# Kernel optimization log

Hardware: AMD Instinct MI355X
Metric: run time of the kernel (lower is better)

## Reference

```python
import jax, jax.numpy as jnp
import numpy as np
from jax import lax

VOCAB = 12000
EMB = 512
RNN = 512
FEATS = 4096
SEQ_LEN = 15


def setup_inputs() -> dict:
    key = jax.random.key(0)
    ks = jax.random.split(key, 10)
    B = 1024
    s = 0.05
    return {
        "img_features": jax.random.normal(ks[0], (B, FEATS), jnp.float32),
        "W_feats": jax.random.normal(ks[1], (EMB, FEATS), jnp.float32) * s,
        "b_feats": jax.random.normal(ks[2], (EMB,), jnp.float32) * s,
        "W_ih": jax.random.normal(ks[3], (4 * RNN, EMB), jnp.float32) * s,
        "W_hh": jax.random.normal(ks[4], (4 * RNN, RNN), jnp.float32) * s,
        "b_ih": jax.random.normal(ks[5], (4 * RNN,), jnp.float32) * s,
        "b_hh": jax.random.normal(ks[6], (4 * RNN,), jnp.float32) * s,
        "emb": jax.random.normal(ks[7], (VOCAB, EMB), jnp.float32) * s,
        "W_out": jax.random.normal(ks[8], (VOCAB - 2, RNN), jnp.float32) * s,
        "b_out": jax.random.normal(ks[9], (VOCAB - 2,), jnp.float32) * s,
    }


def reference(img_features, W_feats, b_feats, W_ih, W_hh, b_ih, b_hh, emb, W_out, b_out):
    B = img_features.shape[0]

    def lstm_cell(x, h, c):
        # torch.nn.LSTMCell: gates ordered i, f, g, o
        gates = x @ W_ih.T + b_ih + h @ W_hh.T + b_hh
        i, f, g, o = jnp.split(gates, 4, axis=1)
        c_new = jax.nn.sigmoid(f) * c + jax.nn.sigmoid(i) * jnp.tanh(g)
        h_new = jax.nn.sigmoid(o) * jnp.tanh(c_new)
        return h_new, c_new

    # image feature embedding + ReLU, then prime the LSTM with it
    img_vec = jax.nn.relu(img_features @ W_feats.T + b_feats)  # [B, 512]
    h = jnp.zeros((B, RNN), img_features.dtype)
    c = jnp.zeros((B, RNN), img_features.dtype)
    h, c = lstm_cell(img_vec, h, c)

    def step(carry, _):
        h, c, words = carry
        x = emb[words]                     # [B, 512] embedding lookup
        h, c = lstm_cell(x, h, c)
        logits = h @ W_out.T + b_out       # [B, VOCAB-2]
        idx = jnp.argmax(logits, axis=1).astype(jnp.int32)
        return (h, c, idx + 2), idx

    words0 = jnp.ones((B,), jnp.int32)  # START token = 1
    _, seq = lax.scan(step, (h, c, words0), None, length=SEQ_LEN)
    return seq.T  # [B, SEQ_LEN] greedy-decoded token ids
```

## Files before the change

### kernel.cpp

```cpp
#include <hip/hip_runtime.h>
#include <stdint.h>

#define BATCH  1024
#define SEQLEN 15
#define NGATE  2048
#define NVOCAB 11998
#define FEATS  4096

typedef __attribute__((ext_vector_type(8)))  short  s8v;
typedef __attribute__((ext_vector_type(16))) float  f32x16;
typedef __attribute__((ext_vector_type(8)))  unsigned short us8;

__device__ __forceinline__ unsigned short f2bf(float f) {
    unsigned u = __float_as_uint(f);
    u += 0x7FFFu + ((u >> 16) & 1u);
    return (unsigned short)(u >> 16);
}
__device__ __forceinline__ float bf2f(unsigned short h) {
    return __uint_as_float(((unsigned)h) << 16);
}
struct bfpair { unsigned short hi, lo; };
__device__ __forceinline__ bfpair split2v(float v) {
    bfpair r;
    r.hi = f2bf(v);
    r.lo = f2bf(v - bf2f(r.hi));
    return r;
}
__device__ __forceinline__ void split8(const float* __restrict__ s, us8& vh, us8& vl) {
    #pragma unroll
    for (int e = 0; e < 8; ++e) {
        bfpair q = split2v(s[e]);
        vh[e] = q.hi; vl[e] = q.lo;
    }
}

__device__ __forceinline__ void async_cp16(const void* g, void* l) {
    __builtin_amdgcn_global_load_lds(
        (const __attribute__((address_space(1))) unsigned int*)g,
        (__attribute__((address_space(3))) unsigned int*)l, 16, 0, 0);
}

__global__ void prep_wcat_blk(const float* __restrict__ W_ih, const float* __restrict__ W_hh,
                              const float* __restrict__ b_ih, const float* __restrict__ b_hh,
                              unsigned short* __restrict__ hi, unsigned short* __restrict__ lo,
                              float* __restrict__ bsum) {
    int idx = blockIdx.x * 256 + threadIdx.x;
    int kc = idx >> 11, row = idx & 2047;
    int k = kc << 3;
    const float* src = (k < 512) ? (W_ih + (size_t)row * 512 + k)
                                 : (W_hh + (size_t)row * 512 + (k - 512));
    us8 vh, vl; split8(src, vh, vl);
    *(us8*)(hi + (size_t)idx * 8) = vh;
    *(us8*)(lo + (size_t)idx * 8) = vl;
    if (idx < NGATE) bsum[idx] = b_ih[idx] + b_hh[idx];
}

__global__ void prep_blk(const float* __restrict__ src,
                         unsigned short* __restrict__ hi, unsigned short* __restrict__ lo,
                         int R, int K) {
    int row = blockIdx.x * 256 + threadIdx.x;
    if (row >= R) return;
    int kc = blockIdx.y;
    us8 vh, vl; split8(src + (size_t)row * K + (kc << 3), vh, vl);
    size_t o = ((size_t)kc * R + row) * 8;
    *(us8*)(hi + o) = vh;
    *(us8*)(lo + o) = vl;
}

__device__ __forceinline__ void mfma_blk_store(
    const unsigned short* __restrict__ Ahi, const unsigned short* __restrict__ Alo, int aRows,
    const unsigned short* __restrict__ Bhi, const unsigned short* __restrict__ Blo, int bRows,
    float* __restrict__ C, int ldc,
    int K, size_t akstride, size_t bkstride, size_t czstride)
{
    __shared__ short smem[4 * 4 * 128 * 8];
    short* sAhi = smem;
    short* sAlo = smem + 4 * 128 * 8;
    short* sBhi = smem + 2 * 4 * 128 * 8;
    short* sBlo = smem + 3 * 4 * 128 * 8;

    const int kz = blockIdx.z;
    Ahi += (size_t)kz * akstride;  Alo += (size_t)kz * akstride;
    Bhi += (size_t)kz * bkstride;  Blo += (size_t)kz * bkstride;
    C   += (size_t)kz * czstride;

    const int tid  = threadIdx.x;
    const int lane = tid & 63, wave = tid >> 6;
    const int wr = (wave & 1) * 64, wc = (wave >> 1) * 64;
    const int col = lane & 31, kh = lane >> 5;
    const int bm = blockIdx.y * 128, bn = blockIdx.x * 128;

    f32x16 acc[2][2] = {};

    for (int k0 = 0; k0 < K; k0 += 32) {
        const int kc0 = k0 >> 3;
        __syncthreads();
        #pragma unroll
        for (int p = 0; p < 2; ++p) {
            int s    = p * 4 + wave;
            int kc_l = s >> 1, rh = s & 1;
            int rl   = rh * 64 + lane;
            int lo_  = (kc_l * 128 + rh * 64) * 8;
            size_t ga = ((size_t)(kc0 + kc_l) * aRows + (bm + rl)) * 8;
            async_cp16(Ahi + ga, sAhi + lo_);
            async_cp16(Alo + ga, sAlo + lo_);
            int brow = bn + rl; if (brow > bRows - 1) brow = bRows - 1;
            size_t gb = ((size_t)(kc0 + kc_l) * bRows + brow) * 8;
            async_cp16(Bhi + gb, sBhi + lo_);
            async_cp16(Blo + gb, sBlo + lo_);
        }
        __syncthreads();

        #pragma unroll
        for (int st = 0; st < 2; ++st) {
            int off = (2 * st + kh) * 128 * 8;
            s8v ah0 = *(const s8v*)(sAhi + off + (wr + col) * 8);
            s8v ah1 = *(const s8v*)(sAhi + off + (wr + 32 + col) * 8);
            s8v al0 = *(const s8v*)(sAlo + off + (wr + col) * 8);
            s8v al1 = *(const s8v*)(sAlo + off + (wr + 32 + col) * 8);
            s8v bh0 = *(const s8v*)(sBhi + off + (wc + col) * 8);
            s8v bh1 = *(const s8v*)(sBhi + off + (wc + 32 + col) * 8);
            s8v bl0 = *(const s8v*)(sBlo + off + (wc + col) * 8);
            s8v bl1 = *(const s8v*)(sBlo + off + (wc + 32 + col) * 8);
            acc[0][0] = __builtin_amdgcn_mfma_f32_32x32x16_bf16(ah0, bh0, acc[0][0], 0, 0, 0);
            acc[0][1] = __builtin_amdgcn_mfma_f32_32x32x16_bf16(ah0, bh1, acc[0][1], 0, 0, 0);
            acc[1][0] = __builtin_amdgcn_mfma_f32_32x32x16_bf16(ah1, bh0, acc[1][0], 0, 0, 0);
            acc[1][1] = __builtin_amdgcn_mfma_f32_32x32x16_bf16(ah1, bh1, acc[1][1], 0, 0, 0);
            acc[0][0] = __builtin_amdgcn_mfma_f32_32x32x16_bf16(ah0, bl0, acc[0][0], 0, 0, 0);
            acc[0][1] = __builtin_amdgcn_mfma_f32_32x32x16_bf16(ah0, bl1, acc[0][1], 0, 0, 0);
            acc[1][0] = __builtin_amdgcn_mfma_f32_32x32x16_bf16(ah1, bl0, acc[1][0], 0, 0, 0);
            acc[1][1] = __builtin_amdgcn_mfma_f32_32x32x16_bf16(ah1, bl1, acc[1][1], 0, 0, 0);
            acc[0][0] = __builtin_amdgcn_mfma_f32_32x32x16_bf16(al0, bh0, acc[0][0], 0, 0, 0);
            acc[0][1] = __builtin_amdgcn_mfma_f32_32x32x16_bf16(al0, bh1, acc[0][1], 0, 0, 0);
            acc[1][0] = __builtin_amdgcn_mfma_f32_32x32x16_bf16(al1, bh0, acc[1][0], 0, 0, 0);
            acc[1][1] = __builtin_amdgcn_mfma_f32_32x32x16_bf16(al1, bh1, acc[1][1], 0, 0, 0);
        }
    }

    #pragma unroll
    for (int i = 0; i < 2; ++i)
        #pragma unroll
        for (int rg = 0; rg < 4; ++rg)
            #pragma unroll
            for (int rr = 0; rr < 4; ++rr) {
                int reg = rg * 4 + rr;
                int m = bm + wr + i * 32 + rr + rg * 8 + kh * 4;
                #pragma unroll
                for (int j = 0; j < 2; ++j) {
                    int n = bn + wc + j * 32 + col;
                    if (n < bRows) C[(size_t)m * ldc + n] = acc[i][j][reg];
                }
            }
}

__global__ __launch_bounds__(256) void k_gemm_gates(
    const unsigned short* Ahi, const unsigned short* Alo,
    const unsigned short* Bhi, const unsigned short* Blo,
    float* C, size_t aks, size_t bks, size_t czs) {
    mfma_blk_store(Ahi, Alo, 1024, Bhi, Blo, NGATE, C, NGATE, 512, aks, bks, czs);
}
__global__ __launch_bounds__(256) void k_gemm_feats(
    const unsigned short* Ahi, const unsigned short* Alo,
    const unsigned short* Bhi, const unsigned short* Blo,
    float* C) {
    mfma_blk_store(Ahi, Alo, 1024, Bhi, Blo, 512, C, 512, 512,
                   (size_t)64 * 1024 * 8, (size_t)64 * 512 * 8, (size_t)1024 * 512);
}

__global__ __launch_bounds__(128, 2) void k_logits_argmax(
    const unsigned short* __restrict__ h_hi, const unsigned short* __restrict__ h_lo,
    const unsigned short* __restrict__ wout_hi, const unsigned short* __restrict__ wout_lo,
    const float* __restrict__ bias, unsigned long long* __restrict__ packed) {
    __shared__ short smem[4 * 4 * 128 * 8];
    short* sAhi = smem;
    short* sAlo = smem + 4096;
    short* sBhi = smem + 8192;
    short* sBlo = smem + 12288;

    const int tid = threadIdx.x;
    const int lane = tid & 63, wave = tid >> 6;
    const int wr = wave * 64;
    const int col = lane & 31, kh = lane >> 5;
    const int bm = blockIdx.y * 128, bn = blockIdx.x * 128;
    const int aRows = 1024, bRows = NVOCAB;

    f32x16 acc[2][4] = {};

    for (int k0 = 0; k0 < 512; k0 += 32) {
        const int kc0 = k0 >> 3;
        __syncthreads();
        #pragma unroll
        for (int p = 0; p < 16; ++p) {
            int s = p * 2 + wave;
            int arr = s >> 3, rem = s & 7;
            int kc_l = rem >> 1, rh = rem & 1;
            int rl = rh * 64 + lane;
            int lo_ = (kc_l * 128 + rh * 64) * 8;
            if (arr < 2) {
                size_t ga = ((size_t)(kc0 + kc_l) * aRows + (bm + rl)) * 8;
                async_cp16((arr == 0 ? h_hi : h_lo) + ga, (arr == 0 ? sAhi : sAlo) + lo_);
            } else {
                int brow = bn + rl; if (brow > bRows - 1) brow = bRows - 1;
                size_t gb = ((size_t)(kc0 + kc_l) * bRows + brow) * 8;
                async_cp16((arr == 2 ? wout_hi : wout_lo) + gb, (arr == 2 ? sBhi : sBlo) + lo_);
            }
        }
        __syncthreads();

        #pragma unroll
        for (int st = 0; st < 2; ++st) {
            int off = (2 * st + kh) * 128 * 8;
            s8v ah0 = *(const s8v*)(sAhi + off + (wr + col) * 8);
            s8v ah1 = *(const s8v*)(sAhi + off + (wr + 32 + col) * 8);
            s8v al0 = *(const s8v*)(sAlo + off + (wr + col) * 8);
            s8v al1 = *(const s8v*)(sAlo + off + (wr + 32 + col) * 8);
            #pragma unroll
            for (int j = 0; j < 4; ++j) {
                s8v bh = *(const s8v*)(sBhi + off + (j * 32 + col) * 8);
                s8v bl = *(const s8v*)(sBlo + off + (j * 32 + col) * 8);
                acc[0][j] = __builtin_amdgcn_mfma_f32_32x32x16_bf16(ah0, bh, acc[0][j], 0, 0, 0);
                acc[1][j] = __builtin_amdgcn_mfma_f32_32x32x16_bf16(ah1, bh, acc[1][j], 0, 0, 0);
                acc[0][j] = __builtin_amdgcn_mfma_f32_32x32x16_bf16(ah0, bl, acc[0][j], 0, 0, 0);
                acc[1][j] = __builtin_amdgcn_mfma_f32_32x32x16_bf16(ah1, bl, acc[1][j], 0, 0, 0);
                acc[0][j] = __builtin_amdgcn_mfma_f32_32x32x16_bf16(al0, bh, acc[0][j], 0, 0, 0);
                acc[1][j] = __builtin_amdgcn_mfma_f32_32x32x16_bf16(al1, bh, acc[1][j], 0, 0, 0);
            }
        }
    }

    #pragma unroll
    for (int i = 0; i < 2; ++i)
        #pragma unroll
        for (int rg = 0; rg < 4; ++rg)
            #pragma unroll
            for (int rr = 0; rr < 4; ++rr) {
                int reg = rg * 4 + rr;
                int m = bm + wr + i * 32 + rr + rg * 8 + kh * 4;
                unsigned long long best = 0ull;
                #pragma unroll
                for (int j = 0; j < 4; ++j) {
                    int n = bn + j * 32 + col;
                    if (n < bRows) {
                        float v = acc[i][j][reg] + bias[n];
                        unsigned int u   = __float_as_uint(v);
                        unsigned int key = (u & 0x80000000u) ? ~u : (u | 0x80000000u);
                        unsigned long long pk =
                            ((unsigned long long)key << 32) |
                            (unsigned long long)(0xFFFFFFFFu - (unsigned)n);
                        best = (pk > best) ? pk : best;
                    }
                }
                #pragma unroll
                for (int sdist = 1; sdist < 32; sdist <<= 1) {
                    unsigned long long o = __shfl_xor(best, sdist, 64);
                    best = (o > best) ? o : best;
                }
                if (col == 0) atomicMax(&packed[m], best);
            }
}

__global__ void feats_reduce8(const float* __restrict__ part, const float* __restrict__ bias,
                              unsigned short* __restrict__ hi, unsigned short* __restrict__ lo) {
    int idx = blockIdx.x * 256 + threadIdx.x;
    int b = idx >> 6, kc = idx & 63;
    int n = kc << 3;
    float v[8];
    #pragma unroll
    for (int e = 0; e < 8; ++e) v[e] = bias[n + e];
    #pragma unroll
    for (int z = 0; z < 8; ++z) {
        const float* s = part + (size_t)z * 1024 * 512 + (size_t)b * 512 + n;
        #pragma unroll
        for (int e = 0; e < 8; ++e) v[e] += s[e];
    }
    us8 vh, vl;
    #pragma unroll
    for (int e = 0; e < 8; ++e) {
        bfpair q = split2v(fmaxf(v[e], 0.f));
        vh[e] = q.hi; vl[e] = q.lo;
    }
    size_t o = ((size_t)kc * 1024 + b) * 8;
    *(us8*)(hi + o) = vh;
    *(us8*)(lo + o) = vl;
}

template<bool PRIME>
__global__ void lstm_pw_blk(const float* __restrict__ g0, const float* __restrict__ g1,
                            const float* __restrict__ bsum, float* __restrict__ cbuf,
                            unsigned short* __restrict__ xh_hi, unsigned short* __restrict__ xh_lo,
                            unsigned long long* __restrict__ packed,
                            int* __restrict__ out, int t) {
    int idx = blockIdx.x * 256 + threadIdx.x;
    int b = idx >> 6, j8 = idx & 63;
    int j = j8 << 3;
    const float* g = g0 + (size_t)b * NGATE;
    float v[4][8];
    #pragma unroll
    for (int gt = 0; gt < 4; ++gt) {
        const float* s = g + gt * 512 + j;
        const float* bs = bsum + gt * 512 + j;
        #pragma unroll
        for (int e = 0; e < 8; ++e) v[gt][e] = s[e] + bs[e];
    }
    if (!PRIME) {
        const float* h2 = g1 + (size_t)b * NGATE;
        #pragma unroll
        for (int gt = 0; gt < 4; ++gt) {
            const float* s = h2 + gt * 512 + j;
            #pragma unroll
            for (int e = 0; e < 8; ++e) v[gt][e] += s[e];
        }
    }
    float* cb = cbuf + (size_t)b * 512 + j;
    us8 vh, vl;
    #pragma unroll
    for (int e = 0; e < 8; ++e) {
        float si = 1.f / (1.f + expf(-v[0][e]));
        float sf = 1.f / (1.f + expf(-v[1][e]));
        float tg = tanhf(v[2][e]);
        float so = 1.f / (1.f + expf(-v[3][e]));
        float cn = PRIME ? (si * tg) : (sf * cb[e] + si * tg);
        cb[e] = cn;
        bfpair q = split2v(so * tanhf(cn));
        vh[e] = q.hi; vl[e] = q.lo;
    }
    size_t o = ((size_t)(64 + j8) * 1024 + b) * 8;
    *(us8*)(xh_hi + o) = vh;
    *(us8*)(xh_lo + o) = vl;
    if (j8 == 0) {
        if (!PRIME && t > 0) {
            unsigned long long p = packed[b];
            out[b * SEQLEN + (t - 1)] = (int)(0xFFFFFFFFu - (unsigned)(p & 0xFFFFFFFFull));
        }
        packed[b] = 0ull;
    }
}

template<int FIRST>
__global__ void gather_blk(const float* __restrict__ emb,
                           const unsigned long long* __restrict__ packed,
                           unsigned short* __restrict__ xh_hi, unsigned short* __restrict__ xh_lo) {
    int idx = blockIdx.x * 256 + threadIdx.x;
    int b = idx >> 6, kc = idx & 63;
    int word = 1;
    if (!FIRST) {
        unsigned long long p = packed[b];
        word = (int)(0xFFFFFFFFu - (unsigned)(p & 0xFFFFFFFFull)) + 2;
    }
    us8 vh, vl; split8(emb + (size_t)word * 512 + (kc << 3), vh, vl);
    size_t o = ((size_t)kc * 1024 + b) * 8;
    *(us8*)(xh_hi + o) = vh;
    *(us8*)(xh_lo + o) = vl;
}

__global__ void final_out(const unsigned long long* __restrict__ packed, int* __restrict__ out) {
    int b = blockIdx.x * 256 + threadIdx.x;
    if (b < BATCH) {
        unsigned long long p = packed[b];
        out[b * SEQLEN + (SEQLEN - 1)] = (int)(0xFFFFFFFFu - (unsigned)(p & 0xFFFFFFFFull));
    }
}

extern "C" void kernel_launch(void* const* d_in, const int* in_sizes, int n_in,
                              void* d_out, int out_size, void* d_ws, size_t ws_size,
                              hipStream_t stream) {
    const float* img     = (const float*)d_in[0];
    const float* W_feats = (const float*)d_in[1];
    const float* b_feats = (const float*)d_in[2];
    const float* W_ih    = (const float*)d_in[3];
    const float* W_hh    = (const float*)d_in[4];
    const float* b_ih    = (const float*)d_in[5];
    const float* b_hh    = (const float*)d_in[6];
    const float* emb     = (const float*)d_in[7];
    const float* W_out   = (const float*)d_in[8];
    const float* b_out   = (const float*)d_in[9];
    int* out = (int*)d_out;

    const size_t WCAT_H = (size_t)128 * 2048 * 8;
    const size_t WOUT_H = (size_t)64 * NVOCAB * 8;
    const size_t XH_H   = (size_t)128 * 1024 * 8;
    const size_t IMGV_H = (size_t)64 * 1024 * 8;

    char* p = (char*)d_ws;
    unsigned short* wcat_hi = (unsigned short*)p;  p += WCAT_H * 2;
    unsigned short* wcat_lo = (unsigned short*)p;  p += WCAT_H * 2;
    unsigned short* wout_hi = (unsigned short*)p;  p += WOUT_H * 2;
    unsigned short* wout_lo = (unsigned short*)p;  p += WOUT_H * 2;
    unsigned short* xh_hi   = (unsigned short*)p;  p += XH_H * 2;
    unsigned short* xh_lo   = (unsigned short*)p;  p += XH_H * 2;
    unsigned short* imgv_hi = (unsigned short*)p;  p += IMGV_H * 2;
    unsigned short* imgv_lo = (unsigned short*)p;  p += IMGV_H * 2;
    float* cbuf             = (float*)p;           p += (size_t)1024 * 512 * 4;
    float* bsum             = (float*)p;           p += (size_t)NGATE * 4;
    unsigned long long* packed = (unsigned long long*)p;  p += (size_t)1024 * 8;
    float* gates0           = (float*)p;           p += (size_t)1024 * NGATE * 4;
    float* gates1           = (float*)p;           p += (size_t)1024 * NGATE * 4;
    unsigned short* imgb_hi = wout_hi;
    unsigned short* imgb_lo = imgb_hi + (size_t)512 * 1024 * 8;
    unsigned short* wfb_hi  = imgb_lo + (size_t)512 * 1024 * 8;
    unsigned short* wfb_lo  = wfb_hi  + (size_t)512 * 512 * 8;
    float* partials = gates0;

    prep_wcat_blk<<<1024, 256, 0, stream>>>(W_ih, W_hh, b_ih, b_hh, wcat_hi, wcat_lo, bsum);
    prep_blk<<<dim3(4, 512), 256, 0, stream>>>(img,     imgb_hi, imgb_lo, 1024, FEATS);
    prep_blk<<<dim3(2, 512), 256, 0, stream>>>(W_feats, wfb_hi,  wfb_lo,  512,  FEATS);

    k_gemm_feats<<<dim3(4, 8, 8), 256, 0, stream>>>(imgb_hi, imgb_lo, wfb_hi, wfb_lo, partials);
    feats_reduce8<<<256, 256, 0, stream>>>(partials, b_feats, imgv_hi, imgv_lo);

    prep_blk<<<dim3(47, 64), 256, 0, stream>>>(W_out, wout_hi, wout_lo, NVOCAB, 512);

    k_gemm_gates<<<dim3(16, 8, 1), 256, 0, stream>>>(imgv_hi, imgv_lo, wcat_hi, wcat_lo,
                                                     gates0, 0, 0, 0);
    lstm_pw_blk<true><<<256, 256, 0, stream>>>(gates0, nullptr, bsum, cbuf,
                                               xh_hi, xh_lo, packed, out, 0);

    for (int t = 0; t < SEQLEN; ++t) {
        if (t == 0) gather_blk<1><<<256, 256, 0, stream>>>(emb, packed, xh_hi, xh_lo);
        else        gather_blk<0><<<256, 256, 0, stream>>>(emb, packed, xh_hi, xh_lo);
        k_gemm_gates<<<dim3(16, 8, 2), 256, 0, stream>>>(
            xh_hi, xh_lo, wcat_hi, wcat_lo, gates0,
            (size_t)64 * 1024 * 8, (size_t)64 * 2048 * 8, (size_t)1024 * NGATE);
        lstm_pw_blk<false><<<256, 256, 0, stream>>>(gates0, gates1, bsum, cbuf,
                                                    xh_hi, xh_lo, packed, out, t);
        k_logits_argmax<<<dim3(94, 8), 128, 0, stream>>>(
            xh_hi + (size_t)64 * 1024 * 8, xh_lo + (size_t)64 * 1024 * 8,
            wout_hi, wout_lo, b_out, packed);
    }
    final_out<<<4, 256, 0, stream>>>(packed, out);
}
```

Measured before the change: 1.757 ms.

## Unify GEMMs into double-buffered pipeline with A fragments loaded directly from global

Replaces three separate MFMA GEMM kernels with one templated gemm_pipe that double-buffers only the B tile in shared memory. The next K-slice is prefetched asynchronously while MFMAs run on the current one, and A fragments are read straight from global into registers. Block M-tile shrinks to 64 rows and grids double, so there are more blocks and higher occupancy (launch_bounds 256,4), with one barrier per K step instead of two. The trade-off is that A is no longer shared through LDS and each block reloads more B data per output, which raises global traffic. Smaller tiles also mean more atomicMax calls in the argmax epilogue.

```diff
diff --git a/kernel.cpp b/kernel.cpp
--- a/kernel.cpp
+++ b/kernel.cpp
@@ -67,17 +67,15 @@
     *(us8*)(lo + o) = vl;
 }
 
-__device__ __forceinline__ void mfma_blk_store(
+template<int MODE>
+__device__ __forceinline__ void gemm_pipe(
     const unsigned short* __restrict__ Ahi, const unsigned short* __restrict__ Alo, int aRows,
     const unsigned short* __restrict__ Bhi, const unsigned short* __restrict__ Blo, int bRows,
-    float* __restrict__ C, int ldc,
-    int K, size_t akstride, size_t bkstride, size_t czstride)
+    float* __restrict__ C, int ldc, int K,
+    size_t akstride, size_t bkstride, size_t czstride,
+    const float* __restrict__ bias, unsigned long long* __restrict__ packed)
 {
-    __shared__ short smem[4 * 4 * 128 * 8];
-    short* sAhi = smem;
-    short* sAlo = smem + 4 * 128 * 8;
-    short* sBhi = smem + 2 * 4 * 128 * 8;
-    short* sBlo = smem + 3 * 4 * 128 * 8;
+    __shared__ short sB[2][2][4][128][8];
 
     const int kz = blockIdx.z;
     Ahi += (size_t)kz * akstride;  Alo += (size_t)kz * akstride;
@@ -86,162 +84,92 @@
 
     const int tid  = threadIdx.x;
     const int lane = tid & 63, wave = tid >> 6;
-    const int wr = (wave & 1) * 64, wc = (wave >> 1) * 64;
+    const int wm = wave & 1, wn = wave >> 1;
     const int col = lane & 31, kh = lane >> 5;
-    const int bm = blockIdx.y * 128, bn = blockIdx.x * 128;
-
-    f32x16 acc[2][2] = {};
-
-    for (int k0 = 0; k0 < K; k0 += 32) {
-        const int kc0 = k0 >> 3;
+    const int bm = blockIdx.y * 64, bn = blockIdx.x * 128;
+    const int arow = bm + wm * 32 + col;
+
+    f32x16 acc[2] = {};
+
+    const int NK = K >> 5;
+
+    #pragma unroll
+    for (int p = 0; p < 4; ++p) {
+        int s = p * 4 + wave;
+        int arr = s >> 3, kc_l = (s >> 1) & 3, rh = s & 1;
+        int brow = bn + rh * 64 + lane; if (brow > bRows - 1) brow = bRows - 1;
+        size_t gb = ((size_t)kc_l * bRows + brow) * 8;
+        async_cp16((arr ? Blo : Bhi) + gb, &sB[0][arr][kc_l][rh * 64][0]);
+    }
+    __syncthreads();
+
+    int cur = 0;
+    for (int ks = 0; ks < NK; ++ks) {
+        const int kc0 = ks << 2;
+
+        s8v ah[2], al[2];
+        #pragma unroll
+        for (int st = 0; st < 2; ++st) {
+            size_t ao = ((size_t)(kc0 + 2 * st + kh) * aRows + arow) * 8;
+            ah[st] = *(const s8v*)(Ahi + ao);
+            al[st] = *(const s8v*)(Alo + ao);
+        }
+
+        if (ks + 1 < NK) {
+            const int kcn = kc0 + 4;
+            #pragma unroll
+            for (int p = 0; p < 4; ++p) {
+                int s = p * 4 + wave;
+                int arr = s >> 3, kc_l = (s >> 1) & 3, rh = s & 1;
+                int brow = bn + rh * 64 + lane; if (brow > bRows - 1) brow = bRows - 1;
+                size_t gb = ((size_t)(kcn + kc_l) * bRows + brow) * 8;
+                async_cp16((arr ? Blo : Bhi) + gb, &sB[cur ^ 1][arr][kc_l][rh * 64][0]);
+            }
+        }
+
+        #pragma unroll
+        for (int st = 0; st < 2; ++st) {
+            const int kl = 2 * st + kh;
+            #pragma unroll
+            for (int j = 0; j < 2; ++j) {
+                const s8v bh = *(const s8v*)&sB[cur][0][kl][wn * 64 + j * 32 + col][0];
+                const s8v bl = *(const s8v*)&sB[cur][1][kl][wn * 64 + j * 32 + col][0];
+                acc[j] = __builtin_amdgcn_mfma_f32_32x32x16_bf16(ah[st], bh, acc[j], 0, 0, 0);
+                acc[j] = __builtin_amdgcn_mfma_f32_32x32x16_bf16(ah[st], bl, acc[j], 0, 0, 0);
+                acc[j] = __builtin_amdgcn_mfma_f32_32x32x16_bf16(al[st], bh, acc[j], 0, 0, 0);
+            }
+        }
+
         __syncthreads();
-        #pragma unroll
-        for (int p = 0; p < 2; ++p) {
-            int s    = p * 4 + wave;
-            int kc_l = s >> 1, rh = s & 1;
-            int rl   = rh * 64 + lane;
-            int lo_  = (kc_l * 128 + rh * 64) * 8;
-            size_t ga = ((size_t)(kc0 + kc_l) * aRows + (bm + rl)) * 8;
-            async_cp16(Ahi + ga, sAhi + lo_);
-            async_cp16(Alo + ga, sAlo + lo_);
-            int brow = bn + rl; if (brow > bRows - 1) brow = bRows - 1;
-            size_t gb = ((size_t)(kc0 + kc_l) * bRows + brow) * 8;
-            async_cp16(Bhi + gb, sBhi + lo_);
-            async_cp16(Blo + gb, sBlo + lo_);
-        }
-        __syncthreads();
-
-        #pragma unroll
-        for (int st = 0; st < 2; ++st) {
-            int off = (2 * st + kh) * 128 * 8;
-            s8v ah0 = *(const s8v*)(sAhi + off + (wr + col) * 8);
-            s8v ah1 = *(const s8v*)(sAhi + off + (wr + 32 + col) * 8);
-            s8v al0 = *(const s8v*)(sAlo + off + (wr + col) * 8);
-            s8v al1 = *(const s8v*)(sAlo + off + (wr + 32 + col) * 8);
-            s8v bh0 = *(const s8v*)(sBhi + off + (wc + col) * 8);
-            s8v bh1 = *(const s8v*)(sBhi + off + (wc + 32 + col) * 8);
-            s8v bl0 = *(const s8v*)(sBlo + off + (wc + col) * 8);
-            s8v bl1 = *(const s8v*)(sBlo + off + (wc + 32 + col) * 8);
-            acc[0][0] = __builtin_amdgcn_mfma_f32_32x32x16_bf16(ah0, bh0, acc[0][0], 0, 0, 0);
-            acc[0][1] = __builtin_amdgcn_mfma_f32_32x32x16_bf16(ah0, bh1, acc[0][1], 0, 0, 0);
-            acc[1][0] = __builtin_amdgcn_mfma_f32_32x32x16_bf16(ah1, bh0, acc[1][0], 0, 0, 0);
-            acc[1][1] = __builtin_amdgcn_mfma_f32_32x32x16_bf16(ah1, bh1, acc[1][1], 0, 0, 0);
-            acc[0][0] = __builtin_amdgcn_mfma_f32_32x32x16_bf16(ah0, bl0, acc[0][0], 0, 0, 0);
-            acc[0][1] = __builtin_amdgcn_mfma_f32_32x32x16_bf16(ah0, bl1, acc[0][1], 0, 0, 0);
-            acc[1][0] = __builtin_amdgcn_mfma_f32_32x32x16_bf16(ah1, bl0, acc[1][0], 0, 0, 0);
-            acc[1][1] = __builtin_amdgcn_mfma_f32_32x32x16_bf16(ah1, bl1, acc[1][1], 0, 0, 0);
-            acc[0][0] = __builtin_amdgcn_mfma_f32_32x32x16_bf16(al0, bh0, acc[0][0], 0, 0, 0);
-            acc[0][1] = __builtin_amdgcn_mfma_f32_32x32x16_bf16(al0, bh1, acc[0][1], 0, 0, 0);
-            acc[1][0] = __builtin_amdgcn_mfma_f32_32x32x16_bf16(al1, bh0, acc[1][0], 0, 0, 0);
-            acc[1][1] = __builtin_amdgcn_mfma_f32_32x32x16_bf16(al1, bh1, acc[1][1], 0, 0, 0);
-        }
-    }
-
-    #pragma unroll
-    for (int i = 0; i < 2; ++i)
+        cur ^= 1;
+    }
+
+    if (MODE == 0) {
         #pragma unroll
         for (int rg = 0; rg < 4; ++rg)
             #pragma unroll
             for (int rr = 0; rr < 4; ++rr) {
                 int reg = rg * 4 + rr;
-                int m = bm + wr + i * 32 + rr + rg * 8 + kh * 4;
+                int m = bm + wm * 32 + rr + rg * 8 + kh * 4;
                 #pragma unroll
                 for (int j = 0; j < 2; ++j) {
-                    int n = bn + wc + j * 32 + col;
-                    if (n < bRows) C[(size_t)m * ldc + n] = acc[i][j][reg];
+                    int n = bn + wn * 64 + j * 32 + col;
+                    if (n < bRows) C[(size_t)m * ldc + n] = acc[j][reg];
                 }
             }
-}
-
-__global__ __launch_bounds__(256) void k_gemm_gates(
-    const unsigned short* Ahi, const unsigned short* Alo,
-    const unsigned short* Bhi, const unsigned short* Blo,
-    float* C, size_t aks, size_t bks, size_t czs) {
-    mfma_blk_store(Ahi, Alo, 1024, Bhi, Blo, NGATE, C, NGATE, 512, aks, bks, czs);
-}
-__global__ __launch_bounds__(256) void k_gemm_feats(
-    const unsigned short* Ahi, const unsigned short* Alo,
-    const unsigned short* Bhi, const unsigned short* Blo,
-    float* C) {
-    mfma_blk_store(Ahi, Alo, 1024, Bhi, Blo, 512, C, 512, 512,
-                   (size_t)64 * 1024 * 8, (size_t)64 * 512 * 8, (size_t)1024 * 512);
-}
-
-__global__ __launch_bounds__(128, 2) void k_logits_argmax(
-    const unsigned short* __restrict__ h_hi, const unsigned short* __restrict__ h_lo,
-    const unsigned short* __restrict__ wout_hi, const unsigned short* __restrict__ wout_lo,
-    const float* __restrict__ bias, unsigned long long* __restrict__ packed) {
-    __shared__ short smem[4 * 4 * 128 * 8];
-    short* sAhi = smem;
-    short* sAlo = smem + 4096;
-    short* sBhi = smem + 8192;
-    short* sBlo = smem + 12288;
-
-    const int tid = threadIdx.x;
-    const int lane = tid & 63, wave = tid >> 6;
-    const int wr = wave * 64;
-    const int col = lane & 31, kh = lane >> 5;
-    const int bm = blockIdx.y * 128, bn = blockIdx.x * 128;
-    const int aRows = 1024, bRows = NVOCAB;
-
-    f32x16 acc[2][4] = {};
-
-    for (int k0 = 0; k0 < 512; k0 += 32) {
-        const int kc0 = k0 >> 3;
-        __syncthreads();
-        #pragma unroll
-        for (int p = 0; p < 16; ++p) {
-            int s = p * 2 + wave;
-            int arr = s >> 3, rem = s & 7;
-            int kc_l = rem >> 1, rh = rem & 1;
-            int rl = rh * 64 + lane;
-            int lo_ = (kc_l * 128 + rh * 64) * 8;
-            if (arr < 2) {
-                size_t ga = ((size_t)(kc0 + kc_l) * aRows + (bm + rl)) * 8;
-                async_cp16((arr == 0 ? h_hi : h_lo) + ga, (arr == 0 ? sAhi : sAlo) + lo_);
-            } else {
-                int brow = bn + rl; if (brow > bRows - 1) brow = bRows - 1;
-                size_t gb = ((size_t)(kc0 + kc_l) * bRows + brow) * 8;
-                async_cp16((arr == 2 ? wout_hi : wout_lo) + gb, (arr == 2 ? sBhi : sBlo) + lo_);
-            }
-        }
-        __syncthreads();
-
-        #pragma unroll
-        for (int st = 0; st < 2; ++st) {
-            int off = (2 * st + kh) * 128 * 8;
-            s8v ah0 = *(const s8v*)(sAhi + off + (wr + col) * 8);
-            s8v ah1 = *(const s8v*)(sAhi + off + (wr + 32 + col) * 8);
-            s8v al0 = *(const s8v*)(sAlo + off + (wr + col) * 8);
-            s8v al1 = *(const s8v*)(sAlo + off + (wr + 32 + col) * 8);
-            #pragma unroll
-            for (int j = 0; j < 4; ++j) {
-                s8v bh = *(const s8v*)(sBhi + off + (j * 32 + col) * 8);
-                s8v bl = *(const s8v*)(sBlo + off + (j * 32 + col) * 8);
-                acc[0][j] = __builtin_amdgcn_mfma_f32_32x32x16_bf16(ah0, bh, acc[0][j], 0, 0, 0);
-                acc[1][j] = __builtin_amdgcn_mfma_f32_32x32x16_bf16(ah1, bh, acc[1][j], 0, 0, 0);
-                acc[0][j] = __builtin_amdgcn_mfma_f32_32x32x16_bf16(ah0, bl, acc[0][j], 0, 0, 0);
-                acc[1][j] = __builtin_amdgcn_mfma_f32_32x32x16_bf16(ah1, bl, acc[1][j], 0, 0, 0);
-                acc[0][j] = __builtin_amdgcn_mfma_f32_32x32x16_bf16(al0, bh, acc[0][j], 0, 0, 0);
-                acc[1][j] = __builtin_amdgcn_mfma_f32_32x32x16_bf16(al1, bh, acc[1][j], 0, 0, 0);
-            }
-        }
-    }
-
-    #pragma unroll
-    for (int i = 0; i < 2; ++i)
+    } else {
         #pragma unroll
         for (int rg = 0; rg < 4; ++rg)
             #pragma unroll
             for (int rr = 0; rr < 4; ++rr) {
                 int reg = rg * 4 + rr;
-                int m = bm + wr + i * 32 + rr + rg * 8 + kh * 4;
+                int m = bm + wm * 32 + rr + rg * 8 + kh * 4;
                 unsigned long long best = 0ull;
                 #pragma unroll
-                for (int j = 0; j < 4; ++j) {
-                    int n = bn + j * 32 + col;
+                for (int j = 0; j < 2; ++j) {
+                    int n = bn + wn * 64 + j * 32 + col;
                     if (n < bRows) {
-                        float v = acc[i][j][reg] + bias[n];
+                        float v = acc[j][reg] + bias[n];
                         unsigned int u   = __float_as_uint(v);
                         unsigned int key = (u & 0x80000000u) ? ~u : (u | 0x80000000u);
                         unsigned long long pk =
@@ -257,6 +185,30 @@
                 }
                 if (col == 0) atomicMax(&packed[m], best);
             }
+    }
+}
+
+__global__ __launch_bounds__(256, 4) void k_gemm_gates(
+    const unsigned short* Ahi, const unsigned short* Alo,
+    const unsigned short* Bhi, const unsigned short* Blo,
+    float* C, size_t aks, size_t bks, size_t czs) {
+    gemm_pipe<0>(Ahi, Alo, 1024, Bhi, Blo, NGATE, C, NGATE, 512, aks, bks, czs,
+                 nullptr, nullptr);
+}
+__global__ __launch_bounds__(256, 4) void k_gemm_feats(
+    const unsigned short* Ahi, const unsigned short* Alo,
+    const unsigned short* Bhi, const unsigned short* Blo,
+    float* C) {
+    gemm_pipe<0>(Ahi, Alo, 1024, Bhi, Blo, 512, C, 512, 512,
+                 (size_t)64 * 1024 * 8, (size_t)64 * 512 * 8, (size_t)1024 * 512,
+                 nullptr, nullptr);
+}
+__global__ __launch_bounds__(256, 4) void k_logits_argmax(
+    const unsigned short* __restrict__ h_hi, const unsigned short* __restrict__ h_lo,
+    const unsigned short* __restrict__ wout_hi, const unsigned short* __restrict__ wout_lo,
+    const float* __restrict__ bias, unsigned long long* __restrict__ packed) {
+    gemm_pipe<1>(h_hi, h_lo, 1024, wout_hi, wout_lo, NVOCAB, nullptr, 0, 512,
+                 0, 0, 0, bias, packed);
 }
 
 __global__ void feats_reduce8(const float* __restrict__ part, const float* __restrict__ bias,
@@ -405,25 +357,25 @@
     prep_blk<<<dim3(4, 512), 256, 0, stream>>>(img,     imgb_hi, imgb_lo, 1024, FEATS);
     prep_blk<<<dim3(2, 512), 256, 0, stream>>>(W_feats, wfb_hi,  wfb_lo,  512,  FEATS);
 
-    k_gemm_feats<<<dim3(4, 8, 8), 256, 0, stream>>>(imgb_hi, imgb_lo, wfb_hi, wfb_lo, partials);
+    k_gemm_feats<<<dim3(4, 16, 8), 256, 0, stream>>>(imgb_hi, imgb_lo, wfb_hi, wfb_lo, partials);
     feats_reduce8<<<256, 256, 0, stream>>>(partials, b_feats, imgv_hi, imgv_lo);
 
     prep_blk<<<dim3(47, 64), 256, 0, stream>>>(W_out, wout_hi, wout_lo, NVOCAB, 512);
 
-    k_gemm_gates<<<dim3(16, 8, 1), 256, 0, stream>>>(imgv_hi, imgv_lo, wcat_hi, wcat_lo,
-                                                     gates0, 0, 0, 0);
+    k_gemm_gates<<<dim3(16, 16, 1), 256, 0, stream>>>(imgv_hi, imgv_lo, wcat_hi, wcat_lo,
+                                                      gates0, 0, 0, 0);
     lstm_pw_blk<true><<<256, 256, 0, stream>>>(gates0, nullptr, bsum, cbuf,
                                                xh_hi, xh_lo, packed, out, 0);
 
     for (int t = 0; t < SEQLEN; ++t) {
         if (t == 0) gather_blk<1><<<256, 256, 0, stream>>>(emb, packed, xh_hi, xh_lo);
         else        gather_blk<0><<<256, 256, 0, stream>>>(emb, packed, xh_hi, xh_lo);
-        k_gemm_gates<<<dim3(16, 8, 2), 256, 0, stream>>>(
+        k_gemm_gates<<<dim3(16, 16, 2), 256, 0, stream>>>(
             xh_hi, xh_lo, wcat_hi, wcat_lo, gates0,
             (size_t)64 * 1024 * 8, (size_t)64 * 2048 * 8, (size_t)1024 * NGATE);
         lstm_pw_blk<false><<<256, 256, 0, stream>>>(gates0, gates1, bsum, cbuf,
                                                     xh_hi, xh_lo, packed, out, t);
-        k_logits_argmax<<<dim3(94, 8), 128, 0, stream>>>(
+        k_logits_argmax<<<dim3(94, 16), 256, 0, stream>>>(
             xh_hi + (size_t)64 * 1024 * 8, xh_lo + (size_t)64 * 1024 * 8,
             wout_hi, wout_lo, b_out, packed);
     }
```

Result: slower. 2.256 ms (+28.4%).
